# Kernel tuning notes

Measured on AMD Instinct MI355X. Metric: run time of the kernel, lower is better.

## Reference

```python
import jax, jax.numpy as jnp
import numpy as np

B, T, C, H = 4, 2048, 1024, 16
D = C // H  # head_dim = 64


def setup_inputs() -> dict:
    key = jax.random.key(0)
    ks = jax.random.split(key, 4)
    scale = 1.0 / np.sqrt(C)
    return {
        "x": jax.random.normal(ks[0], (B, T, C), dtype=jnp.float32),
        "attn_mask": jnp.ones((B, T), dtype=jnp.int32),
        "W_qkv": jax.random.normal(ks[1], (C, 3 * C), dtype=jnp.float32) * scale,
        "b_qkv": jnp.zeros((3 * C,), dtype=jnp.float32),
        "W_proj": jax.random.normal(ks[2], (C, C), dtype=jnp.float32) * scale,
        "b_proj": jnp.zeros((C,), dtype=jnp.float32),
    }


def reference(x, attn_mask, W_qkv, b_qkv, W_proj, b_proj):
    b, t, c = x.shape
    qkv = x @ W_qkv + b_qkv                      # (B,T,3C)
    q, k, v = jnp.split(qkv, 3, axis=-1)
    # b t (h d) -> b h t d
    q = q.reshape(b, t, H, D).transpose(0, 2, 1, 3)
    k = k.reshape(b, t, H, D).transpose(0, 2, 1, 3)
    v = v.reshape(b, t, H, D).transpose(0, 2, 1, 3)
    att = jnp.einsum("bhtd,bhsd->bhts", q, k) / jnp.sqrt(jnp.float32(D))
    causal = jnp.tril(jnp.ones((t, t), dtype=bool))[None, None]       # (1,1,T,T)
    pad = (attn_mask[:, None, None, :t] != 0)                         # (B,1,1,T)
    att = jnp.where(causal & pad, att, -jnp.inf)
    att = jax.nn.softmax(att, axis=-1)
    y = jnp.einsum("bhts,bhsd->bhtd", att, v)   # (B,H,T,D)
    y = y.transpose(0, 2, 1, 3).reshape(b, t, c)
    return y @ W_proj + b_proj
```

## Files before the change

kernel.cpp:

```cpp
#include <hip/hip_runtime.h>
#include <math.h>

#define B_ 4
#define T_ 2048
#define C_ 1024
#define H_ 16
#define D_ 64
#define M_ (B_*T_)
#define N1_ (3*C_)

typedef __attribute__((ext_vector_type(8))) short bf16x8;
typedef __attribute__((ext_vector_type(4))) short bf16x4;
typedef __attribute__((ext_vector_type(4))) float f32x4;
typedef __attribute__((ext_vector_type(16))) float f32x16;

__device__ __forceinline__ short f2bf(float f){
  union { float f; unsigned u; } v; v.f = f;
  unsigned r = (v.u + 0x7fffu + ((v.u >> 16) & 1u)) >> 16;
  return (short)r;
}

__device__ __forceinline__ unsigned cvtpk(float lo, float hi){
  unsigned r;
  asm("v_cvt_pk_bf16_f32 %0, %1, %2" : "=v"(r) : "v"(lo), "v"(hi));
  return r;
}

__device__ __forceinline__ void plswap(unsigned &a, unsigned &b){
  asm volatile("v_permlane32_swap_b32 %0, %1" : "+v"(a), "+v"(b));
}
__device__ __forceinline__ float xhalf_add(float x){
  unsigned a = __float_as_uint(x), b = a;
  asm volatile("v_permlane32_swap_b32 %0, %1" : "+v"(a), "+v"(b));
  return __uint_as_float(a) + __uint_as_float(b);
}

__device__ __forceinline__ void gll16(const void* g, void* l){
  __builtin_amdgcn_global_load_lds((const __attribute__((address_space(1))) void*)g,
                                   (__attribute__((address_space(3))) void*)l, 16, 0, 0);
}

__global__ __launch_bounds__(256) void convx(const float* __restrict__ x, short* __restrict__ xb, int n){
  int i = (blockIdx.x*256 + threadIdx.x)*8;
  if (i >= n) return;
  float4 a = *(const float4*)(x+i), b = *(const float4*)(x+i+4);
  bf16x8 o;
  o[0]=f2bf(a.x); o[1]=f2bf(a.y); o[2]=f2bf(a.z); o[3]=f2bf(a.w);
  o[4]=f2bf(b.x); o[5]=f2bf(b.y); o[6]=f2bf(b.z); o[7]=f2bf(b.w);
  *(bf16x8*)(xb+i) = o;
}

__global__ __launch_bounds__(256) void transw(const float* __restrict__ W, short* __restrict__ Wt, int K, int N){
  __shared__ float tl[64][72];
  int tid = threadIdx.x;
  int n0 = blockIdx.x*64, k0 = blockIdx.y*64;
  #pragma unroll
  for (int i=0;i<4;i++){
    int row = (tid>>4) + i*16;
    int col4 = (tid&15)*4;
    float4 v = *(const float4*)&W[(size_t)(k0+row)*N + n0 + col4];
    *(float4*)&tl[row][col4] = v;
  }
  __syncthreads();
  #pragma unroll
  for (int i=0;i<2;i++){
    int nr = (tid>>3) + i*32;
    int ch = tid&7;
    bf16x8 o;
    #pragma unroll
    for (int e=0;e<8;e++) o[e] = f2bf(tl[ch*8+e][nr]);
    *(bf16x8*)&Wt[(size_t)(n0+nr)*K + k0 + ch*8] = o;
  }
}

template<int OUTBF>
__global__ __launch_bounds__(512) void gemm_bt(const short* __restrict__ A, const short* __restrict__ Bt,
           const float* __restrict__ bias, short* __restrict__ outb, float* __restrict__ outf,
           int M, int N, int K)
{
  __shared__ __attribute__((aligned(128))) char LDSC[147456];
  const int tid = threadIdx.x;
  const int wv = tid>>6, ln = tid&63;
  const int lnr = ln&15, lg = ln>>4;
  const int wm = wv>>1, wn = wv&1;
  const int nx = gridDim.x;
  const int nwg = nx*gridDim.y;
  const int lin = blockIdx.x + nx*blockIdx.y;
  const int swz = (lin&7)*(nwg>>3) + (lin>>3);
  const int m0 = (swz/nx)*256, n0 = (swz%nx)*128;

  const int srA = tid>>3;
  const int sg  = (tid&7) ^ (srA&7);
  const short* Ag = A  + (size_t)(m0 + srA)*K + sg*8;
  const short* Bg = Bt + (size_t)(n0 + srA)*K + sg*8;

  const int fsw = (lg ^ (lnr&7))<<4;
  const int aln = (wm*64 + lnr)*128 + fsw;
  const int bln = (wn*64 + lnr)*128 + fsw;

  auto STAGE = [&](int kt, int bi){
    const short* a = Ag + kt*64;
    const short* b = Bg + kt*64;
    char* ab = LDSC + bi*32768 + wv*1024;
    char* bb = LDSC + 98304 + bi*16384 + wv*1024;
    gll16(a,                ab);
    gll16(a + (size_t)64*K, ab + 8192);
    gll16(a + (size_t)128*K, ab + 16384);
    gll16(a + (size_t)192*K, ab + 24576);
    gll16(b,                bb);
    gll16(b + (size_t)64*K, bb + 8192);
  };

  f32x4 acc[4][4];
  #pragma unroll
  for (int i=0;i<4;i++)
    #pragma unroll
    for (int j=0;j<4;j++) acc[i][j] = (f32x4){0.f,0.f,0.f,0.f};

  const int NT = K >> 6;
  STAGE(0, 0);
  STAGE(1, 1);
  asm volatile("s_waitcnt vmcnt(6)" ::: "memory");
  __builtin_amdgcn_sched_barrier(0);
  __builtin_amdgcn_s_barrier();
  __builtin_amdgcn_sched_barrier(0);

  int cb = 0, sb = 2;
  #pragma unroll 1
  for (int kt = 0; kt < NT; kt++){
    if (kt + 2 < NT) STAGE(kt + 2, sb);

    const char* ab = LDSC + cb*32768;
    const char* bb = LDSC + 98304 + cb*16384;
    bf16x8 af[4][2], bfr[4][2];
    #pragma unroll
    for (int mi=0;mi<4;mi++)
      #pragma unroll
      for (int ks=0;ks<2;ks++)
        af[mi][ks] = *(const bf16x8*)(ab + ((aln + mi*2048) ^ (ks<<6)));
    #pragma unroll
    for (int ni=0;ni<4;ni++)
      #pragma unroll
      for (int ks=0;ks<2;ks++)
        bfr[ni][ks] = *(const bf16x8*)(bb + ((bln + ni*2048) ^ (ks<<6)));

    __builtin_amdgcn_s_setprio(1);
    #pragma unroll
    for (int mi=0;mi<4;mi++)
      #pragma unroll
      for (int ni=0;ni<4;ni++)
        #pragma unroll
        for (int ks=0;ks<2;ks++)
          acc[mi][ni] = __builtin_amdgcn_mfma_f32_16x16x32_bf16(af[mi][ks], bfr[ni][ks], acc[mi][ni], 0,0,0);
    __builtin_amdgcn_s_setprio(0);

    if (kt < NT-1){
      __builtin_amdgcn_sched_barrier(0);
      if (kt < NT-2){ asm volatile("s_waitcnt vmcnt(6)" ::: "memory"); }
      else          { asm volatile("s_waitcnt vmcnt(0)" ::: "memory"); }
      __builtin_amdgcn_sched_barrier(0);
      __builtin_amdgcn_s_barrier();
      __builtin_amdgcn_sched_barrier(0);
    }
    cb = (cb==2) ? 0 : cb+1;
    sb = (sb==2) ? 0 : sb+1;
  }

  #pragma unroll
  for (int mi=0;mi<4;mi++){
    #pragma unroll
    for (int ni=0;ni<4;ni++){
      int col = n0 + wn*64 + ni*16 + lnr;
      float bv = bias[col];
      #pragma unroll
      for (int r=0;r<4;r++){
        int row = m0 + wm*64 + mi*16 + lg*4 + r;
        float v = acc[mi][ni][r] + bv;
        if (OUTBF) outb[(size_t)row*N + col] = f2bf(v);
        else       outf[(size_t)row*N + col] = v;
      }
    }
  }
}

__global__ __launch_bounds__(256) void transv(const short* __restrict__ qkv, short* __restrict__ vt){
  __shared__ short tl[64][72];
  int tid = threadIdx.x;
  int t0 = blockIdx.x*64, bh = blockIdx.y;
  int b = bh>>4, h = bh&15;
  int tr = tid>>2, cc = (tid&3)*16;
  const short* src = &qkv[(size_t)(b*T_ + t0 + tr)*N1_ + 2*C_ + h*D_ + cc];
  #pragma unroll
  for (int i=0;i<4;i++){
    bf16x4 v = *(const bf16x4*)(src + i*4);
    *(bf16x4*)&tl[tr][cc + i*4] = v;
  }
  __syncthreads();
  int d = tid>>2, tc = (tid&3)*16;
  #pragma unroll
  for (int i=0;i<2;i++){
    bf16x8 o;
    #pragma unroll
    for (int e=0;e<8;e++) o[e] = tl[tc + i*8 + e][d];
    *(bf16x8*)&vt[(size_t)(bh*D_ + d)*T_ + t0 + tc + i*8] = o;
  }
}

__global__ __launch_bounds__(256) void attn9(const short* __restrict__ qkv, const short* __restrict__ vt,
           const int* __restrict__ mask, short* __restrict__ yb)
{
  __shared__ short Ks[2][64*64];
  __shared__ short Vs[2][64*64];
  const int tid = threadIdx.x;
  const int wv = tid>>6, ln = tid&63;
  const int l31 = ln & 31, hi = ln >> 5;
  const int bh = blockIdx.x, b = bh>>4, hd = bh&15;
  const int c = 15 - (int)blockIdx.y;
  const float cexp = 0.18033688f;
  const float MC   = 11.541561f;

  const int srow = tid>>3;
  const int scol = (tid&7) ^ (srow&7);
  const short* kgb = qkv + (size_t)(b*T_ + srow)*N1_ + C_ + hd*D_ + scol*8;
  const short* vgb = vt  + (size_t)((bh<<6) + srow)*T_ + scol*8;
  int fa[4];
  #pragma unroll
  for (int i=0;i<4;i++)
    fa[i] = l31*128 + ((((i<<1)+hi) ^ (l31&7)) << 4);

  const int q0w = c*128 + wv*32;
  const int ntb  = 2*c + 2;
  const int myNt = 2*c + 1 + (wv>>1);

  bf16x8 qf[4];
  const short* qbase = qkv + (size_t)(b*T_ + q0w + l31)*N1_ + hd*D_ + hi*8;
  #pragma unroll
  for (int ds=0; ds<4; ds++) qf[ds] = *(const bf16x8*)(qbase + ds*16);

  f32x16 o0, o1;
  #pragma unroll
  for (int r=0;r<16;r++){ o0[r]=0.f; o1[r]=0.f; }
  float lsum = 0.f;

  int mv_next = mask[b*T_ + ln];
  {
    char* kd = (char*)Ks[0]; char* vd = (char*)Vs[0];
    gll16(kgb,                  kd + wv*1024);
    gll16(kgb + (size_t)32*N1_, kd + 4096 + wv*1024);
    gll16(vgb,                  vd + wv*1024);
    gll16(vgb + (size_t)32*T_,  vd + 4096 + wv*1024);
  }
  __syncthreads();

  #pragma unroll 1
  for (int jt = 0; jt < ntb; jt++){
    const int j0 = jt << 6;
    int mv_cur = mv_next;
    if (jt+1 < ntb){
      mv_next = mask[b*T_ + ((jt+1)<<6) + ln];
      char* kd = (char*)Ks[(jt+1)&1]; char* vd = (char*)Vs[(jt+1)&1];
      const short* kg = kgb + (size_t)((jt+1)<<6)*N1_;
      const short* vg = vgb + ((jt+1)<<6);
      gll16(kg,                  kd + wv*1024);
      gll16(kg + (size_t)32*N1_, kd + 4096 + wv*1024);
      gll16(vg,                  vd + wv*1024);
      gll16(vg + (size_t)32*T_,  vd + 4096 + wv*1024);
    }
    unsigned long long bm = __ballot(mv_cur != 0);

    if (jt < myNt){
      const char* ksb = (const char*)Ks[jt&1];
      const char* vsb = (const char*)Vs[jt&1];
      f32x16 s0, s1;
      #pragma unroll
      for (int r=0;r<16;r++){ s0[r]=0.f; s1[r]=0.f; }
      __builtin_amdgcn_s_setprio(1);
      #pragma unroll
      for (int ds=0; ds<4; ds++){
        bf16x8 k0 = *(const bf16x8*)(ksb + fa[ds]);
        bf16x8 k1 = *(const bf16x8*)(ksb + fa[ds] + 4096);
        s0 = __builtin_amdgcn_mfma_f32_32x32x16_bf16(k0, qf[ds], s0, 0,0,0);
        s1 = __builtin_amdgcn_mfma_f32_32x32x16_bf16(k1, qf[ds], s1, 0,0,0);
      }
      __builtin_amdgcn_s_setprio(0);

      const int qglob = q0w + l31;
      const bool allm = (bm == ~0ull);
      if (!allm){
        #pragma unroll
        for (int r=0;r<16;r++){
          int kr = (r&3) + 8*(r>>2) + 4*hi;
          bool ok0 = (j0 + kr      <= qglob) && ((bm >> kr) & 1);
          bool ok1 = (j0 + kr + 32 <= qglob) && ((bm >> (kr+32)) & 1);
          s0[r] = ok0 ? s0[r] : -INFINITY;
          s1[r] = ok1 ? s1[r] : -INFINITY;
        }
      } else if (j0 + 63 > q0w){
        #pragma unroll
        for (int r=0;r<16;r++){
          int kr = (r&3) + 8*(r>>2) + 4*hi;
          s0[r] = (j0 + kr      <= qglob) ? s0[r] : -INFINITY;
          s1[r] = (j0 + kr + 32 <= qglob) ? s1[r] : -INFINITY;
        }
      }

      #pragma unroll
      for (int r=0;r<16;r++){
        s0[r] = __builtin_amdgcn_exp2f(__builtin_fmaf(s0[r], cexp, -MC));
        s1[r] = __builtin_amdgcn_exp2f(__builtin_fmaf(s1[r], cexp, -MC));
      }
      float u[8];
      #pragma unroll
      for (int i=0;i<8;i++) u[i] = (s0[i]+s0[i+8]) + (s1[i]+s1[i+8]);
      #pragma unroll
      for (int i=0;i<4;i++) u[i] = u[i] + u[i+4];
      float ps = (u[0]+u[1]) + (u[2]+u[3]);
      lsum += xhalf_add(ps);

      unsigned LA[2][4], LB[2][4];
      #pragma unroll
      for (int rq=0; rq<4; rq++){
        LA[0][rq] = cvtpk(s0[4*rq],   s0[4*rq+1]);
        LB[0][rq] = cvtpk(s0[4*rq+2], s0[4*rq+3]);
        LA[1][rq] = cvtpk(s1[4*rq],   s1[4*rq+1]);
        LB[1][rq] = cvtpk(s1[4*rq+2], s1[4*rq+3]);
      }

      #pragma unroll
      for (int kt2=0; kt2<4; kt2++){
        const int kt = kt2>>1, sub = kt2&1;
        bf16x8 v0 = *(const bf16x8*)(vsb + fa[kt2]);
        bf16x8 v1 = *(const bf16x8*)(vsb + fa[kt2] + 4096);
        unsigned a0 = LA[kt][2*sub], a1 = LA[kt][2*sub+1];
        unsigned b0 = LB[kt][2*sub], b1 = LB[kt][2*sub+1];
        plswap(a0, a1);
        plswap(b0, b1);
        union { unsigned u[4]; bf16x8 v; } pf;
        pf.u[0] = a0; pf.u[1] = b0; pf.u[2] = a1; pf.u[3] = b1;
        __builtin_amdgcn_s_setprio(1);
        o0 = __builtin_amdgcn_mfma_f32_32x32x16_bf16(pf.v, v0, o0, 0,0,0);
        o1 = __builtin_amdgcn_mfma_f32_32x32x16_bf16(pf.v, v1, o1, 0,0,0);
        __builtin_amdgcn_s_setprio(0);
      }
    }
    __syncthreads();
  }

  float linv = 1.0f / lsum;
  #pragma unroll
  for (int r=0;r<16;r++){
    int qs = (r&3) + 8*(r>>2) + 4*hi;
    float lv = __shfl(linv, qs);
    size_t base = (size_t)(b*T_ + q0w + qs)*C_ + hd*D_ + l31;
    yb[base]      = f2bf(o0[r]*lv);
    yb[base + 32] = f2bf(o1[r]*lv);
  }
}

extern "C" void kernel_launch(void* const* d_in, const int* in_sizes, int n_in,
                              void* d_out, int out_size, void* d_ws, size_t ws_size,
                              hipStream_t stream){
  const float* x     = (const float*)d_in[0];
  const int*   mask  = (const int*)d_in[1];
  const float* Wqkv  = (const float*)d_in[2];
  const float* bqkv  = (const float*)d_in[3];
  const float* Wproj = (const float*)d_in[4];
  const float* bproj = (const float*)d_in[5];
  float* out = (float*)d_out;

  char* w = (char*)d_ws;
  short* xb     = (short*)w; w += (size_t)M_*C_*2;
  short* wqkvT  = (short*)w; w += (size_t)N1_*C_*2;
  short* wprojT = (short*)w; w += (size_t)C_*C_*2;
  short* qkvb   = (short*)w; w += (size_t)M_*N1_*2;
  short* vtb    = (short*)w; w += (size_t)B_*H_*D_*T_*2;
  short* yb     = (short*)w; w += (size_t)M_*C_*2;

  convx<<<dim3((M_*C_)/(256*8)), 256, 0, stream>>>(x, xb, M_*C_);
  transw<<<dim3(N1_/64, C_/64), 256, 0, stream>>>(Wqkv, wqkvT, C_, N1_);
  transw<<<dim3(C_/64,  C_/64), 256, 0, stream>>>(Wproj, wprojT, C_, C_);
  gemm_bt<1><<<dim3(N1_/128, M_/256), 512, 0, stream>>>(xb, wqkvT, bqkv, qkvb, nullptr, M_, N1_, C_);
  transv<<<dim3(T_/64, B_*H_), 256, 0, stream>>>(qkvb, vtb);
  attn9<<<dim3(B_*H_, 16), 256, 0, stream>>>(qkvb, vtb, mask, yb);
  gemm_bt<0><<<dim3(C_/128, M_/256), 512, 0, stream>>>(yb, wprojT, bproj, nullptr, out, M_, C_, C_);
}
```

Measured before the change: 184.0 us.

## Fold softmax scale into QKV GEMM epilogue and use explicit vmcnt waits in attention

The QKV GEMM epilogue now pre-multiplies the Q columns by the softmax exp2 scale. The attention kernel seeds its score accumulators with -MC, so the per-element FMA before exp2 goes away. The K/V double-buffer pipeline drops __syncthreads in favour of partial s_waitcnt vmcnt plus raw s_barrier, so the next tile's loads stay in flight while the current tile is computed. Scaling Q before bf16 rounding changes numerics slightly, and the hardcoded vmcnt count depends on how many loads are in flight (the next tile's four loads plus the mask load).

After: 182.3 us. No clear change (-1.0%).

```diff
diff --git a/kernel.cpp b/kernel.cpp
--- a/kernel.cpp
+++ b/kernel.cpp
@@ -176,8 +176,12 @@
       for (int r=0;r<4;r++){
         int row = m0 + wm*64 + mi*16 + lg*4 + r;
         float v = acc[mi][ni][r] + bv;
-        if (OUTBF) outb[(size_t)row*N + col] = f2bf(v);
-        else       outf[(size_t)row*N + col] = v;
+        if (OUTBF){
+          if (col < C_) v *= 0.18033688f;
+          outb[(size_t)row*N + col] = f2bf(v);
+        } else {
+          outf[(size_t)row*N + col] = v;
+        }
       }
     }
   }
@@ -206,7 +210,7 @@
   }
 }
 
-__global__ __launch_bounds__(256) void attn9(const short* __restrict__ qkv, const short* __restrict__ vt,
+__global__ __launch_bounds__(256) void attn13(const short* __restrict__ qkv, const short* __restrict__ vt,
            const int* __restrict__ mask, short* __restrict__ yb)
 {
   __shared__ short Ks[2][64*64];
@@ -216,8 +220,7 @@
   const int l31 = ln & 31, hi = ln >> 5;
   const int bh = blockIdx.x, b = bh>>4, hd = bh&15;
   const int c = 15 - (int)blockIdx.y;
-  const float cexp = 0.18033688f;
-  const float MC   = 11.541561f;
+  const float MC = 11.541561f;
 
   const int srow = tid>>3;
   const int scol = (tid&7) ^ (srow&7);
@@ -242,30 +245,35 @@
   for (int r=0;r<16;r++){ o0[r]=0.f; o1[r]=0.f; }
   float lsum = 0.f;
 
-  int mv_next = mask[b*T_ + ln];
-  {
-    char* kd = (char*)Ks[0]; char* vd = (char*)Vs[0];
-    gll16(kgb,                  kd + wv*1024);
-    gll16(kgb + (size_t)32*N1_, kd + 4096 + wv*1024);
-    gll16(vgb,                  vd + wv*1024);
-    gll16(vgb + (size_t)32*T_,  vd + 4096 + wv*1024);
-  }
-  __syncthreads();
+  auto STAGE = [&](int jt){
+    char* kd = (char*)Ks[jt&1]; char* vd = (char*)Vs[jt&1];
+    const short* kg = kgb + (size_t)(jt<<6)*N1_;
+    const short* vg = vgb + (jt<<6);
+    gll16(kg,                  kd + wv*1024);
+    gll16(kg + (size_t)32*N1_, kd + 4096 + wv*1024);
+    gll16(vg,                  vd + wv*1024);
+    gll16(vg + (size_t)32*T_,  vd + 4096 + wv*1024);
+  };
+
+  int mv_cur = mask[b*T_ + ln];
+  STAGE(0);
 
   #pragma unroll 1
   for (int jt = 0; jt < ntb; jt++){
     const int j0 = jt << 6;
-    int mv_cur = mv_next;
+    int mv_nx = 0;
     if (jt+1 < ntb){
-      mv_next = mask[b*T_ + ((jt+1)<<6) + ln];
-      char* kd = (char*)Ks[(jt+1)&1]; char* vd = (char*)Vs[(jt+1)&1];
-      const short* kg = kgb + (size_t)((jt+1)<<6)*N1_;
-      const short* vg = vgb + ((jt+1)<<6);
-      gll16(kg,                  kd + wv*1024);
-      gll16(kg + (size_t)32*N1_, kd + 4096 + wv*1024);
-      gll16(vg,                  vd + wv*1024);
-      gll16(vg + (size_t)32*T_,  vd + 4096 + wv*1024);
+      mv_nx = mask[b*T_ + ((jt+1)<<6) + ln];
+      STAGE(jt+1);
+      __builtin_amdgcn_sched_barrier(0);
+      asm volatile("s_waitcnt vmcnt(5)" ::: "memory");
+    } else {
+      __builtin_amdgcn_sched_barrier(0);
+      asm volatile("s_waitcnt vmcnt(0)" ::: "memory");
     }
+    __builtin_amdgcn_sched_barrier(0);
+    __builtin_amdgcn_s_barrier();
+    __builtin_amdgcn_sched_barrier(0);
     unsigned long long bm = __ballot(mv_cur != 0);
 
     if (jt < myNt){
@@ -273,7 +281,7 @@
       const char* vsb = (const char*)Vs[jt&1];
       f32x16 s0, s1;
       #pragma unroll
-      for (int r=0;r<16;r++){ s0[r]=0.f; s1[r]=0.f; }
+      for (int r=0;r<16;r++){ s0[r]=-MC; s1[r]=-MC; }
       __builtin_amdgcn_s_setprio(1);
       #pragma unroll
       for (int ds=0; ds<4; ds++){
@@ -306,8 +314,8 @@
 
       #pragma unroll
       for (int r=0;r<16;r++){
-        s0[r] = __builtin_amdgcn_exp2f(__builtin_fmaf(s0[r], cexp, -MC));
-        s1[r] = __builtin_amdgcn_exp2f(__builtin_fmaf(s1[r], cexp, -MC));
+        s0[r] = __builtin_amdgcn_exp2f(s0[r]);
+        s1[r] = __builtin_amdgcn_exp2f(s1[r]);
       }
       float u[8];
       #pragma unroll
@@ -343,7 +351,10 @@
         __builtin_amdgcn_s_setprio(0);
       }
     }
-    __syncthreads();
+    __builtin_amdgcn_sched_barrier(0);
+    __builtin_amdgcn_s_barrier();
+    __builtin_amdgcn_sched_barrier(0);
+    mv_cur = mv_nx;
   }
 
   float linv = 1.0f / lsum;
@@ -381,6 +392,6 @@
   transw<<<dim3(C_/64,  C_/64), 256, 0, stream>>>(Wproj, wprojT, C_, C_);
   gemm_bt<1><<<dim3(N1_/128, M_/256), 512, 0, stream>>>(xb, wqkvT, bqkv, qkvb, nullptr, M_, N1_, C_);
   transv<<<dim3(T_/64, B_*H_), 256, 0, stream>>>(qkvb, vtb);
-  attn9<<<dim3(B_*H_, 16), 256, 0, stream>>>(qkvb, vtb, mask, yb);
+  attn13<<<dim3(B_*H_, 16), 256, 0, stream>>>(qkvb, vtb, mask, yb);
   gemm_bt<0><<<dim3(C_/128, M_/256), 512, 0, stream>>>(yb, wprojT, bproj, nullptr, out, M_, C_, C_);
 }
```
